# Kernel tuning notes

Measured on AMD Instinct MI355X. Metric: run time of the kernel, lower is better.

Reference implementation:

```python
import jax, jax.numpy as jnp
import numpy as np

B, S, DM, H = 4, 2048, 512, 8
HD = DM // H


def setup_inputs() -> dict:
    key = jax.random.key(0)
    ks = jax.random.split(key, 12)
    x = jax.random.normal(ks[0], (B, S, DM), dtype=jnp.float32)
    # causal lower-triangular mask [B, S, S]
    mask = jnp.broadcast_to(jnp.tril(jnp.ones((S, S), dtype=jnp.int32)), (B, S, S))
    # sorted irregular day offsets (trading-day-like), in days
    days_offset = jnp.sort(
        jax.random.uniform(ks[1], (B, S), dtype=jnp.float32) * 3000.0, axis=-1
    )
    scale = 1.0 / np.sqrt(DM)
    Wq = jax.random.normal(ks[2], (DM, DM), dtype=jnp.float32) * scale
    bq = jnp.zeros((DM,), dtype=jnp.float32)
    Wk = jax.random.normal(ks[3], (DM, DM), dtype=jnp.float32) * scale
    bk = jnp.zeros((DM,), dtype=jnp.float32)
    Wv = jax.random.normal(ks[4], (DM, DM), dtype=jnp.float32) * scale
    bv = jnp.zeros((DM,), dtype=jnp.float32)
    Wo = jax.random.normal(ks[5], (DM, DM), dtype=jnp.float32) * scale
    bo = jnp.zeros((DM,), dtype=jnp.float32)
    decay_rate = jnp.float32(0.1)
    return {
        "x": x, "mask": mask, "days_offset": days_offset,
        "Wq": Wq, "bq": bq, "Wk": Wk, "bk": bk,
        "Wv": Wv, "bv": bv, "Wo": Wo, "bo": bo,
        "decay_rate": decay_rate,
    }


def reference(x, mask, days_offset, Wq, bq, Wk, bk, Wv, bv, Wo, bo, decay_rate):
    b, s, _ = x.shape
    # projections (torch Linear: x @ W.T + b), split heads -> [b, h, s, hd]
    def proj(W, bias):
        return (x @ W.T + bias).reshape(b, s, H, HD).transpose(0, 2, 1, 3)
    q, k, v = proj(Wq, bq), proj(Wk, bk), proj(Wv, bv)
    scores = jnp.einsum("bhqd,bhkd->bhqk", q, k) / jnp.sqrt(jnp.float32(HD))
    # temporal decay: exp(-rate * |t_i - t_j|), broadcast over heads
    dist = jnp.abs(days_offset[:, :, None] - days_offset[:, None, :])  # [b,s,s]
    decay = jnp.exp(-decay_rate * dist)
    scores = scores * decay[:, None, :, :]
    scores = jnp.where(mask[:, None, :, :] == 0, -jnp.inf, scores)
    attn = jax.nn.softmax(scores, axis=-1)  # dropout p=0 (eval)
    out = jnp.einsum("bhqk,bhkd->bhqd", attn, v)
    out = out.transpose(0, 2, 1, 3).reshape(b, s, DM)
    return out @ Wo.T + bo
```

## Files before the change

### kernel.cpp

```cpp
#include <hip/hip_runtime.h>
#include <hip/hip_fp16.h>


#define S_LEN 2048
#define DMODEL 512
#define NH 8
#define HD 64

typedef _Float16 half8 __attribute__((ext_vector_type(8)));
typedef _Float16 half4 __attribute__((ext_vector_type(4)));
typedef float floatx4 __attribute__((ext_vector_type(4)));

__device__ __forceinline__ void gload16(const _Float16* g, _Float16* l) {
    __builtin_amdgcn_global_load_lds(
        (const __attribute__((address_space(1))) void*)g,
        (__attribute__((address_space(3))) void*)l, 16, 0, 0);
}

__global__ __launch_bounds__(256) void cast_f2h(
    const float* __restrict__ x,
    const float* __restrict__ Wq, const float* __restrict__ Wk,
    const float* __restrict__ Wv, const float* __restrict__ Wo,
    _Float16* __restrict__ xh, _Float16* __restrict__ Wh)
{
    const int z = blockIdx.y;
    const float* src;
    _Float16* dst;
    int n;
    if (z == 0) { src = x; dst = xh; n = 8192 * 512; }
    else {
        src = (z == 1) ? Wq : (z == 2) ? Wk : (z == 3) ? Wv : Wo;
        dst = Wh + (z - 1) * 262144;
        n = 262144;
    }
    const int stride = gridDim.x * 256 * 4;
    for (int i = (blockIdx.x * 256 + threadIdx.x) * 4; i < n; i += stride) {
        float4 v = *(const float4*)(src + i);
        half4 h;
        h[0] = (_Float16)v.x; h[1] = (_Float16)v.y;
        h[2] = (_Float16)v.z; h[3] = (_Float16)v.w;
        *(half4*)(dst + i) = h;
    }
}

__global__ __launch_bounds__(256) void qkv_gemm(
    const _Float16* __restrict__ xh, const _Float16* __restrict__ Wh,
    const float* __restrict__ bq, const float* __restrict__ bk, const float* __restrict__ bv,
    _Float16* __restrict__ outh)
{
    __shared__ _Float16 As[2][128 * 64];
    __shared__ _Float16 Ws[2][128 * 64];
    const int t = threadIdx.x;
    const int bm = blockIdx.x, bn = blockIdx.y, z = blockIdx.z;
    const float* bias = (z == 0) ? bq : (z == 1) ? bk : bv;
    const int w = t >> 6, lane = t & 63, l15 = lane & 15, quad = lane >> 4;
    const int wrow = (w >> 1) * 64, wcol = (w & 1) * 64;
    const int lrow = lane >> 3, lane7 = lane & 7;
    const int sw = lane7 ^ lrow;
    const _Float16* xb = xh + (size_t)(bm * 128) * DMODEL;
    const _Float16* Wb = Wh + z * 262144 + (size_t)(bn * 128) * DMODEL;

    auto stage = [&](int kb, int buf) {
        #pragma unroll
        for (int i = 0; i < 4; ++i) {
            const int grp = w * 4 + i;
            const int row = grp * 8 + lrow;
            gload16(xb + (size_t)row * DMODEL + kb * 64 + sw * 8, &As[buf][grp * 512]);
            gload16(Wb + (size_t)row * DMODEL + kb * 64 + sw * 8, &Ws[buf][grp * 512]);
        }
    };

    floatx4 acc[4][4] = {};
    stage(0, 0);
    for (int kb = 0; kb < 8; ++kb) {
        const int buf = kb & 1;
        __syncthreads();
        if (kb < 7) stage(kb + 1, buf ^ 1);
        #pragma unroll
        for (int kk = 0; kk < 2; ++kk) {
            half8 xf[4], wf[4];
            #pragma unroll
            for (int mt = 0; mt < 4; ++mt)
                xf[mt] = *(const half8*)(&As[buf][(wrow + mt * 16 + l15) * 64 + (((quad + 4 * kk) ^ (l15 & 7)) * 8)]);
            #pragma unroll
            for (int nt = 0; nt < 4; ++nt)
                wf[nt] = *(const half8*)(&Ws[buf][(wcol + nt * 16 + l15) * 64 + (((quad + 4 * kk) ^ (l15 & 7)) * 8)]);
            if (z == 2) {
                #pragma unroll
                for (int mt = 0; mt < 4; ++mt)
                    #pragma unroll
                    for (int nt = 0; nt < 4; ++nt)
                        acc[mt][nt] = __builtin_amdgcn_mfma_f32_16x16x32_f16(xf[mt], wf[nt], acc[mt][nt], 0, 0, 0);
            } else {
                #pragma unroll
                for (int nt = 0; nt < 4; ++nt)
                    #pragma unroll
                    for (int mt = 0; mt < 4; ++mt)
                        acc[nt][mt] = __builtin_amdgcn_mfma_f32_16x16x32_f16(wf[nt], xf[mt], acc[nt][mt], 0, 0, 0);
            }
        }
    }

    if (z == 2) {
        #pragma unroll
        for (int mt = 0; mt < 4; ++mt)
            #pragma unroll
            for (int nt = 0; nt < 4; ++nt) {
                int n = bn * 128 + wcol + nt * 16 + l15;
                float bvv = bias[n];
                int m0 = bm * 128 + wrow + mt * 16 + quad * 4;
                int b = m0 >> 11, s0 = m0 & 2047;
                int hh = n >> 6, hd = n & 63;
                half4 hv;
                #pragma unroll
                for (int r = 0; r < 4; ++r) hv[r] = (_Float16)(acc[mt][nt][r] + bvv);
                *(half4*)(outh + (size_t)2 * (8192 * 512) +
                          ((size_t)(b * NH + hh) * HD + hd) * S_LEN + s0) = hv;
            }
    } else {
        #pragma unroll
        for (int nt = 0; nt < 4; ++nt)
            #pragma unroll
            for (int mt = 0; mt < 4; ++mt) {
                int n0 = bn * 128 + wcol + nt * 16 + quad * 4;
                float4 b4 = *(const float4*)(bias + n0);
                int m = bm * 128 + wrow + mt * 16 + l15;
                int b = m >> 11, s = m & 2047;
                int hh = n0 >> 6, hd0 = n0 & 63;
                half4 hv;
                hv[0] = (_Float16)(acc[nt][mt][0] + b4.x);
                hv[1] = (_Float16)(acc[nt][mt][1] + b4.y);
                hv[2] = (_Float16)(acc[nt][mt][2] + b4.z);
                hv[3] = (_Float16)(acc[nt][mt][3] + b4.w);
                *(half4*)(outh + (size_t)z * (8192 * 512) +
                          ((size_t)(b * NH + hh) * S_LEN + s) * HD + hd0) = hv;
            }
    }
}

__global__ __launch_bounds__(256) void out_gemm(
    const _Float16* __restrict__ A, const _Float16* __restrict__ Woh,
    const float* __restrict__ bo, float* __restrict__ outf)
{
    __shared__ _Float16 As[2][64 * 64];
    __shared__ _Float16 Ws[2][128 * 64];
    const int t = threadIdx.x;
    const int bm = blockIdx.x, bn = blockIdx.y;
    const int w = t >> 6, lane = t & 63, l15 = lane & 15, quad = lane >> 4;
    const int wn = w * 32;
    const int lrow = lane >> 3, lane7 = lane & 7;
    const int sw = lane7 ^ lrow;
    const _Float16* Ab = A   + (size_t)(bm * 64) * DMODEL;
    const _Float16* Wb = Woh + (size_t)(bn * 128) * DMODEL;

    auto stage = [&](int kb, int buf) {
        #pragma unroll
        for (int i = 0; i < 2; ++i) {
            const int grp = w * 2 + i;
            const int row = grp * 8 + lrow;
            gload16(Ab + (size_t)row * DMODEL + kb * 64 + sw * 8, &As[buf][grp * 512]);
        }
        #pragma unroll
        for (int i = 0; i < 4; ++i) {
            const int grp = w * 4 + i;
            const int row = grp * 8 + lrow;
            gload16(Wb + (size_t)row * DMODEL + kb * 64 + sw * 8, &Ws[buf][grp * 512]);
        }
    };

    floatx4 acc[2][4] = {};
    stage(0, 0);
    for (int kb = 0; kb < 8; ++kb) {
        const int buf = kb & 1;
        __syncthreads();
        if (kb < 7) stage(kb + 1, buf ^ 1);
        #pragma unroll
        for (int kk = 0; kk < 2; ++kk) {
            half8 wf[2], af[4];
            #pragma unroll
            for (int nt = 0; nt < 2; ++nt)
                wf[nt] = *(const half8*)(&Ws[buf][(wn + nt * 16 + l15) * 64 + (((quad + 4 * kk) ^ (l15 & 7)) * 8)]);
            #pragma unroll
            for (int mt = 0; mt < 4; ++mt)
                af[mt] = *(const half8*)(&As[buf][(mt * 16 + l15) * 64 + (((quad + 4 * kk) ^ (l15 & 7)) * 8)]);
            #pragma unroll
            for (int nt = 0; nt < 2; ++nt)
                #pragma unroll
                for (int mt = 0; mt < 4; ++mt)
                    acc[nt][mt] = __builtin_amdgcn_mfma_f32_16x16x32_f16(wf[nt], af[mt], acc[nt][mt], 0, 0, 0);
        }
    }

    #pragma unroll
    for (int nt = 0; nt < 2; ++nt)
        #pragma unroll
        for (int mt = 0; mt < 4; ++mt) {
            int n0 = bn * 128 + wn + nt * 16 + quad * 4;
            float4 b4 = *(const float4*)(bo + n0);
            int m = bm * 64 + mt * 16 + l15;
            float4 v;
            v.x = acc[nt][mt][0] + b4.x; v.y = acc[nt][mt][1] + b4.y;
            v.z = acc[nt][mt][2] + b4.z; v.w = acc[nt][mt][3] + b4.w;
            *(float4*)(outf + (size_t)m * DMODEL + n0) = v;
        }
}

__global__ __launch_bounds__(256, 2) void attn_k(
    const _Float16* __restrict__ Qh, const _Float16* __restrict__ Kh,
    const _Float16* __restrict__ Vt, const float* __restrict__ days,
    const float* __restrict__ rate_p, _Float16* __restrict__ Ah)
{
    __shared__ _Float16 Ks[2][64 * 64];
    __shared__ _Float16 Vs[2][64 * 64];
    __shared__ float    eks[2][64];
    __shared__ float4   PsRaw[1024];
    __shared__ float    lred[2][2][64];

    _Float16* Ps  = (_Float16*)PsRaw;
    float*    PsF = (float*)PsRaw;

    const int h = blockIdx.x, pr = blockIdx.y, b = blockIdx.z;
    const int t = threadIdx.x, w = t >> 6, lane = t & 63;
    const int l15 = lane & 15, quad = lane >> 4, e7 = l15 & 7;
    const int qh = w & 1, kh = w >> 1;
    const float rate = rate_p[0];
    const size_t bhoff = (size_t)(b * NH + h) * (size_t)(S_LEN * HD);
    const _Float16* Qb = Qh + bhoff;
    const _Float16* Kb = Kh + bhoff;
    const _Float16* Vb = Vt + bhoff;
    const float* daysb = days + b * S_LEN;
    const int lrow = lane >> 3, sw = (lane & 7) ^ lrow;

    auto stage = [&](int kt, int buf) {
        #pragma unroll
        for (int i = 0; i < 2; ++i) {
            int grp = w * 2 + i;
            int row = grp * 8 + lrow;
            gload16(Kb + (size_t)(kt * 64 + row) * HD + sw * 8, &Ks[buf][grp * 512]);
            gload16(Vb + (size_t)row * S_LEN + kt * 64 + sw * 8, &Vs[buf][grp * 512]);
        }
        if (w == 0) {
            float tk0 = daysb[kt * 64];
            float d = daysb[kt * 64 + lane];
            eks[buf][lane] = __expf(fminf(rate * (d - tk0), 80.f));
        }
    };

    auto run_phase = [&](int j, int par0, int nextj) -> int {
        const int q0 = j * 64 + qh * 32;
        half8 qf[2][2];
        #pragma unroll
        for (int qc = 0; qc < 2; ++qc)
            #pragma unroll
            for (int kk = 0; kk < 2; ++kk)
                qf[qc][kk] = *(const half8*)(Qb + (size_t)(q0 + qc * 16 + l15) * HD + kk * 32 + quad * 8);

        const int   qg[2] = {q0 + l15, q0 + 16 + l15};
        const float tq[2] = {daysb[qg[0]], daysb[qg[1]]};

        floatx4 oacc[2][4] = {};
        float lacc[2] = {0.f, 0.f};

        floatx4 scA[2][2], scB[2][2];
        half8  vfA[4], vfB[4];
        floatx4 ekA[2], ekB[2];
        float  eqA[2], eqB[2];

        auto load_tile = [&](int kt, int par, floatx4 (&sc)[2][2], half8 (&vf)[4],
                             floatx4 (&ek)[2], float (&eq)[2]) {
            half8 kf[2][2];
            #pragma unroll
            for (int c = 0; c < 2; ++c) {
                const int C = kh * 2 + c;
                #pragma unroll
                for (int kk = 0; kk < 2; ++kk)
                    kf[c][kk] = *(const half8*)(&Ks[par][(C * 16 + l15) * 64 + (((quad + 4 * kk) ^ e7) * 8)]);
            }
            #pragma unroll
            for (int qc = 0; qc < 2; ++qc)
                #pragma unroll
                for (int c = 0; c < 2; ++c) {
                    floatx4 z = {};
                    z = __builtin_amdgcn_mfma_f32_16x16x32_f16(kf[c][0], qf[qc][0], z, 0, 0, 0);
                    sc[qc][c] = __builtin_amdgcn_mfma_f32_16x16x32_f16(kf[c][1], qf[qc][1], z, 0, 0, 0);
                }
            #pragma unroll
            for (int s4 = 0; s4 < 4; ++s4)
                vf[s4] = *(const half8*)(&Vs[par][(s4 * 16 + l15) * 64 + (((quad + 4 * kh) ^ e7) * 8)]);
            const float tk0 = daysb[kt * 64];
            #pragma unroll
            for (int qc = 0; qc < 2; ++qc)
                eq[qc] = 0.125f * __expf(-rate * (tq[qc] - tk0));
            #pragma unroll
            for (int c = 0; c < 2; ++c)
                ek[c] = *(const floatx4*)(&eks[par][kh * 32 + c * 16 + quad * 4]);
        };

        auto softmax_pv = [&](floatx4 (&sc)[2][2], half8 (&vf)[4],
                              floatx4 (&ek)[2], float (&eq)[2], bool dg, int kt) {
            #pragma unroll
            for (int qc = 0; qc < 2; ++qc)
                #pragma unroll
                for (int c = 0; c < 2; ++c) {
                    float pv[4];
                    #pragma unroll
                    for (int r = 0; r < 4; ++r) {
                        float p = __expf(sc[qc][c][r] * (eq[qc] * ek[c][r]));
                        if (dg && (kt * 64 + kh * 32 + c * 16 + quad * 4 + r) > qg[qc]) p = 0.f;
                        lacc[qc] += p;
                        pv[r] = p;
                    }
                    half4 hv;
                    hv[0] = (_Float16)pv[0]; hv[1] = (_Float16)pv[1];
                    hv[2] = (_Float16)pv[2]; hv[3] = (_Float16)pv[3];
                    *(half4*)(&Ps[(w * 2 + qc) * 1024 + l15 * 64 +
                                  (((kh * 4 + 2 * c + (quad >> 1)) ^ e7) * 8) + (quad & 1) * 4]) = hv;
                }
            #pragma unroll
            for (int qc = 0; qc < 2; ++qc) {
                half8 pf = *(const half8*)(&Ps[(w * 2 + qc) * 1024 + l15 * 64 + (((quad + 4 * kh) ^ e7) * 8)]);
                #pragma unroll
                for (int s4 = 0; s4 < 4; ++s4)
                    oacc[qc][s4] = __builtin_amdgcn_mfma_f32_16x16x32_f16(vf[s4], pf, oacc[qc][s4], 0, 0, 0);
            }
        };

        __syncthreads();
        if (j > 0) stage(1, par0 ^ 1);
        load_tile(0, par0, scA, vfA, ekA, eqA);

        int kt = 1;
        for (; kt + 1 <= j; kt += 2) {
            const int p1 = (par0 + kt) & 1;
            __syncthreads();
            if (kt < j) stage(kt + 1, p1 ^ 1);
            load_tile(kt, p1, scB, vfB, ekB, eqB);
            softmax_pv(scA, vfA, ekA, eqA, false, kt - 1);
            const int p2 = p1 ^ 1;
            __syncthreads();
            if (kt + 1 < j) stage(kt + 2, p2 ^ 1);
            load_tile(kt + 1, p2, scA, vfA, ekA, eqA);
            softmax_pv(scB, vfB, ekB, eqB, false, kt);
        }
        if (kt <= j) {
            const int p1 = (par0 + kt) & 1;
            __syncthreads();
            load_tile(kt, p1, scB, vfB, ekB, eqB);
            softmax_pv(scA, vfA, ekA, eqA, false, kt - 1);
            softmax_pv(scB, vfB, ekB, eqB, true, j);
        } else {
            softmax_pv(scA, vfA, ekA, eqA, true, j);
        }

        __syncthreads();
        if (w >= 2) {
            #pragma unroll
            for (int qc = 0; qc < 2; ++qc) {
                #pragma unroll
                for (int s4 = 0; s4 < 4; ++s4)
                    *(floatx4*)(&PsF[(((w & 1) * 2 + qc) * 4 + s4) * 256 + lane * 4]) = oacc[qc][s4];
                lred[w & 1][qc][lane] = lacc[qc];
            }
        }
        __syncthreads();
        const int parNext = (par0 + j + 1) & 1;
        if (nextj >= 0) stage(0, parNext);
        if (w < 2) {
            #pragma unroll
            for (int qc = 0; qc < 2; ++qc) {
                float l = lacc[qc] + lred[w][qc][lane];
                l += __shfl_xor(l, 16);
                l += __shfl_xor(l, 32);
                const float linv = 1.0f / l;
                #pragma unroll
                for (int s4 = 0; s4 < 4; ++s4) {
                    floatx4 o = oacc[qc][s4] +
                        *(const floatx4*)(&PsF[((w * 2 + qc) * 4 + s4) * 256 + lane * 4]);
                    half4 hv;
                    #pragma unroll
                    for (int r = 0; r < 4; ++r) hv[r] = (_Float16)(o[r] * linv);
                    *(half4*)(Ah + ((size_t)(b * S_LEN) + qg[qc]) * DMODEL + h * HD + s4 * 16 + quad * 4) = hv;
                }
            }
        }
        return parNext;
    };

    const int j0 = pr, j1 = 31 - pr;
    stage(0, 0);
    int p1 = run_phase(j0, 0, j1);
    run_phase(j1, p1, -1);
}

extern "C" void kernel_launch(void* const* d_in, const int* in_sizes, int n_in,
                              void* d_out, int out_size, void* d_ws, size_t ws_size,
                              hipStream_t stream)
{
    const float* x    = (const float*)d_in[0];
    const float* days = (const float*)d_in[2];
    const float* Wq   = (const float*)d_in[3];
    const float* bq   = (const float*)d_in[4];
    const float* Wk   = (const float*)d_in[5];
    const float* bk   = (const float*)d_in[6];
    const float* Wv   = (const float*)d_in[7];
    const float* bv   = (const float*)d_in[8];
    const float* Wo   = (const float*)d_in[9];
    const float* bo   = (const float*)d_in[10];
    const float* rate = (const float*)d_in[11];
    float* out = (float*)d_out;

    _Float16* Qh  = (_Float16*)d_ws;
    _Float16* Kh  = Qh + 4194304;
    _Float16* Vh  = Kh + 4194304;
    _Float16* AhX = Vh + 4194304;
    _Float16* Wh  = AhX + 4194304;

    dim3 gc(512, 5, 1);
    cast_f2h<<<gc, 256, 0, stream>>>(x, Wq, Wk, Wv, Wo, AhX, Wh);

    dim3 g0(64, 4, 3);
    qkv_gemm<<<g0, 256, 0, stream>>>(AhX, Wh, bq, bk, bv, Qh);

    dim3 ga(NH, 16, 4);
    attn_k<<<ga, 256, 0, stream>>>(Qh, Kh, Vh, days, rate, AhX);

    dim3 g1(128, 4, 1);
    out_gemm<<<g1, 256, 0, stream>>>(AhX, Wh + 3 * 262144, bo, out);
}
```

Baseline: 203.3 us.

## Use 512-thread blocks covering 128 query rows, dropping paired-phase load balancing

After: 331.6 us. +63.1%, slower.

```diff
diff --git a/kernel.cpp b/kernel.cpp
--- a/kernel.cpp
+++ b/kernel.cpp
@@ -205,7 +205,7 @@
         }
 }
 
-__global__ __launch_bounds__(256, 2) void attn_k(
+__global__ __launch_bounds__(512, 4) void attn_k(
     const _Float16* __restrict__ Qh, const _Float16* __restrict__ Kh,
     const _Float16* __restrict__ Vt, const float* __restrict__ days,
     const float* __restrict__ rate_p, _Float16* __restrict__ Ah)
@@ -213,16 +213,18 @@
     __shared__ _Float16 Ks[2][64 * 64];
     __shared__ _Float16 Vs[2][64 * 64];
     __shared__ float    eks[2][64];
-    __shared__ float4   PsRaw[1024];
-    __shared__ float    lred[2][2][64];
+    __shared__ float4   PsRaw[2048];
+    __shared__ float    lred[4][2][64];
 
     _Float16* Ps  = (_Float16*)PsRaw;
     float*    PsF = (float*)PsRaw;
 
-    const int h = blockIdx.x, pr = blockIdx.y, b = blockIdx.z;
+    const int h = blockIdx.x, b = blockIdx.y;
+    const int j = 15 - blockIdx.z;
     const int t = threadIdx.x, w = t >> 6, lane = t & 63;
     const int l15 = lane & 15, quad = lane >> 4, e7 = l15 & 7;
-    const int qh = w & 1, kh = w >> 1;
+    const int qq = w >> 1, kh = w & 1;
+    const int nt = 2 * j + 2;
     const float rate = rate_p[0];
     const size_t bhoff = (size_t)(b * NH + h) * (size_t)(S_LEN * HD);
     const _Float16* Qb = Qh + bhoff;
@@ -232,13 +234,9 @@
     const int lrow = lane >> 3, sw = (lane & 7) ^ lrow;
 
     auto stage = [&](int kt, int buf) {
-        #pragma unroll
-        for (int i = 0; i < 2; ++i) {
-            int grp = w * 2 + i;
-            int row = grp * 8 + lrow;
-            gload16(Kb + (size_t)(kt * 64 + row) * HD + sw * 8, &Ks[buf][grp * 512]);
-            gload16(Vb + (size_t)row * S_LEN + kt * 64 + sw * 8, &Vs[buf][grp * 512]);
-        }
+        const int row = w * 8 + lrow;
+        gload16(Kb + (size_t)(kt * 64 + row) * HD + sw * 8, &Ks[buf][w * 512]);
+        gload16(Vb + (size_t)row * S_LEN + kt * 64 + sw * 8, &Vs[buf][w * 512]);
         if (w == 0) {
             float tk0 = daysb[kt * 64];
             float d = daysb[kt * 64 + lane];
@@ -246,150 +244,139 @@
         }
     };
 
-    auto run_phase = [&](int j, int par0, int nextj) -> int {
-        const int q0 = j * 64 + qh * 32;
-        half8 qf[2][2];
+    const int q0 = j * 128 + qq * 32;
+    half8 qf[2][2];
+    #pragma unroll
+    for (int qc = 0; qc < 2; ++qc)
+        #pragma unroll
+        for (int kk = 0; kk < 2; ++kk)
+            qf[qc][kk] = *(const half8*)(Qb + (size_t)(q0 + qc * 16 + l15) * HD + kk * 32 + quad * 8);
+
+    const int   qg[2] = {q0 + l15, q0 + 16 + l15};
+    const float tq[2] = {daysb[qg[0]], daysb[qg[1]]};
+
+    floatx4 oacc[2][4] = {};
+    float lacc[2] = {0.f, 0.f};
+
+    floatx4 scA[2][2], scB[2][2];
+    half8  vfA[4], vfB[4];
+    floatx4 ekA[2], ekB[2];
+    float  eqA[2], eqB[2];
+
+    auto load_tile = [&](int kt, int par, floatx4 (&sc)[2][2], half8 (&vf)[4],
+                         floatx4 (&ek)[2], float (&eq)[2]) {
+        half8 kf[2][2];
+        #pragma unroll
+        for (int c = 0; c < 2; ++c) {
+            const int C = kh * 2 + c;
+            #pragma unroll
+            for (int kk = 0; kk < 2; ++kk)
+                kf[c][kk] = *(const half8*)(&Ks[par][(C * 16 + l15) * 64 + (((quad + 4 * kk) ^ e7) * 8)]);
+        }
         #pragma unroll
         for (int qc = 0; qc < 2; ++qc)
             #pragma unroll
-            for (int kk = 0; kk < 2; ++kk)
-                qf[qc][kk] = *(const half8*)(Qb + (size_t)(q0 + qc * 16 + l15) * HD + kk * 32 + quad * 8);
-
-        const int   qg[2] = {q0 + l15, q0 + 16 + l15};
-        const float tq[2] = {daysb[qg[0]], daysb[qg[1]]};
-
-        floatx4 oacc[2][4] = {};
-        float lacc[2] = {0.f, 0.f};
-
-        floatx4 scA[2][2], scB[2][2];
-        half8  vfA[4], vfB[4];
-        floatx4 ekA[2], ekB[2];
-        float  eqA[2], eqB[2];
-
-        auto load_tile = [&](int kt, int par, floatx4 (&sc)[2][2], half8 (&vf)[4],
-                             floatx4 (&ek)[2], float (&eq)[2]) {
-            half8 kf[2][2];
-            #pragma unroll
             for (int c = 0; c < 2; ++c) {
-                const int C = kh * 2 + c;
-                #pragma unroll
-                for (int kk = 0; kk < 2; ++kk)
-                    kf[c][kk] = *(const half8*)(&Ks[par][(C * 16 + l15) * 64 + (((quad + 4 * kk) ^ e7) * 8)]);
-            }
-            #pragma unroll
-            for (int qc = 0; qc < 2; ++qc)
-                #pragma unroll
-                for (int c = 0; c < 2; ++c) {
-                    floatx4 z = {};
-                    z = __builtin_amdgcn_mfma_f32_16x16x32_f16(kf[c][0], qf[qc][0], z, 0, 0, 0);
-                    sc[qc][c] = __builtin_amdgcn_mfma_f32_16x16x32_f16(kf[c][1], qf[qc][1], z, 0, 0, 0);
+                floatx4 z = {};
+                z = __builtin_amdgcn_mfma_f32_16x16x32_f16(kf[c][0], qf[qc][0], z, 0, 0, 0);
+                sc[qc][c] = __builtin_amdgcn_mfma_f32_16x16x32_f16(kf[c][1], qf[qc][1], z, 0, 0, 0);
+            }
+        #pragma unroll
+        for (int s4 = 0; s4 < 4; ++s4)
+            vf[s4] = *(const half8*)(&Vs[par][(s4 * 16 + l15) * 64 + (((quad + 4 * kh) ^ e7) * 8)]);
+        const float tk0 = daysb[kt * 64];
+        #pragma unroll
+        for (int qc = 0; qc < 2; ++qc)
+            eq[qc] = 0.125f * __expf(-rate * (tq[qc] - tk0));
+        #pragma unroll
+        for (int c = 0; c < 2; ++c)
+            ek[c] = *(const floatx4*)(&eks[par][kh * 32 + c * 16 + quad * 4]);
+    };
+
+    auto softmax_pv = [&](floatx4 (&sc)[2][2], half8 (&vf)[4],
+                          floatx4 (&ek)[2], float (&eq)[2], bool dg, int kt) {
+        #pragma unroll
+        for (int qc = 0; qc < 2; ++qc)
+            #pragma unroll
+            for (int c = 0; c < 2; ++c) {
+                float pv[4];
+                #pragma unroll
+                for (int r = 0; r < 4; ++r) {
+                    float p = __expf(sc[qc][c][r] * (eq[qc] * ek[c][r]));
+                    if (dg && (kt * 64 + kh * 32 + c * 16 + quad * 4 + r) > qg[qc]) p = 0.f;
+                    lacc[qc] += p;
+                    pv[r] = p;
                 }
+                half4 hv;
+                hv[0] = (_Float16)pv[0]; hv[1] = (_Float16)pv[1];
+                hv[2] = (_Float16)pv[2]; hv[3] = (_Float16)pv[3];
+                *(half4*)(&Ps[(w * 2 + qc) * 1024 + l15 * 64 +
+                              (((kh * 4 + 2 * c + (quad >> 1)) ^ e7) * 8) + (quad & 1) * 4]) = hv;
+            }
+        #pragma unroll
+        for (int qc = 0; qc < 2; ++qc) {
+            half8 pf = *(const half8*)(&Ps[(w * 2 + qc) * 1024 + l15 * 64 + (((quad + 4 * kh) ^ e7) * 8)]);
             #pragma unroll
             for (int s4 = 0; s4 < 4; ++s4)
-                vf[s4] = *(const half8*)(&Vs[par][(s4 * 16 + l15) * 64 + (((quad + 4 * kh) ^ e7) * 8)]);
-            const float tk0 = daysb[kt * 64];
-            #pragma unroll
-            for (int qc = 0; qc < 2; ++qc)
-                eq[qc] = 0.125f * __expf(-rate * (tq[qc] - tk0));
-            #pragma unroll
-            for (int c = 0; c < 2; ++c)
-                ek[c] = *(const floatx4*)(&eks[par][kh * 32 + c * 16 + quad * 4]);
-        };
-
-        auto softmax_pv = [&](floatx4 (&sc)[2][2], half8 (&vf)[4],
-                              floatx4 (&ek)[2], float (&eq)[2], bool dg, int kt) {
-            #pragma unroll
-            for (int qc = 0; qc < 2; ++qc)
-                #pragma unroll
-                for (int c = 0; c < 2; ++c) {
-                    float pv[4];
-                    #pragma unroll
-                    for (int r = 0; r < 4; ++r) {
-                        float p = __expf(sc[qc][c][r] * (eq[qc] * ek[c][r]));
-                        if (dg && (kt * 64 + kh * 32 + c * 16 + quad * 4 + r) > qg[qc]) p = 0.f;
-                        lacc[qc] += p;
-                        pv[r] = p;
-                    }
-                    half4 hv;
-                    hv[0] = (_Float16)pv[0]; hv[1] = (_Float16)pv[1];
-                    hv[2] = (_Float16)pv[2]; hv[3] = (_Float16)pv[3];
-                    *(half4*)(&Ps[(w * 2 + qc) * 1024 + l15 * 64 +
-                                  (((kh * 4 + 2 * c + (quad >> 1)) ^ e7) * 8) + (quad & 1) * 4]) = hv;
-                }
-            #pragma unroll
-            for (int qc = 0; qc < 2; ++qc) {
-                half8 pf = *(const half8*)(&Ps[(w * 2 + qc) * 1024 + l15 * 64 + (((quad + 4 * kh) ^ e7) * 8)]);
-                #pragma unroll
-                for (int s4 = 0; s4 < 4; ++s4)
-                    oacc[qc][s4] = __builtin_amdgcn_mfma_f32_16x16x32_f16(vf[s4], pf, oacc[qc][s4], 0, 0, 0);
-            }
-        };
-
+                oacc[qc][s4] = __builtin_amdgcn_mfma_f32_16x16x32_f16(vf[s4], pf, oacc[qc][s4], 0, 0, 0);
+        }
+    };
+
+    stage(0, 0);
+    __syncthreads();
+    if (nt > 1) stage(1, 1);
+    load_tile(0, 0, scA, vfA, ekA, eqA);
+
+    int kt = 1;
+    for (; kt + 1 < nt; kt += 2) {
+        const int p1 = kt & 1;
         __syncthreads();
-        if (j > 0) stage(1, par0 ^ 1);
-        load_tile(0, par0, scA, vfA, ekA, eqA);
-
-        int kt = 1;
-        for (; kt + 1 <= j; kt += 2) {
-            const int p1 = (par0 + kt) & 1;
-            __syncthreads();
-            if (kt < j) stage(kt + 1, p1 ^ 1);
-            load_tile(kt, p1, scB, vfB, ekB, eqB);
-            softmax_pv(scA, vfA, ekA, eqA, false, kt - 1);
-            const int p2 = p1 ^ 1;
-            __syncthreads();
-            if (kt + 1 < j) stage(kt + 2, p2 ^ 1);
-            load_tile(kt + 1, p2, scA, vfA, ekA, eqA);
-            softmax_pv(scB, vfB, ekB, eqB, false, kt);
-        }
-        if (kt <= j) {
-            const int p1 = (par0 + kt) & 1;
-            __syncthreads();
-            load_tile(kt, p1, scB, vfB, ekB, eqB);
-            softmax_pv(scA, vfA, ekA, eqA, false, kt - 1);
-            softmax_pv(scB, vfB, ekB, eqB, true, j);
-        } else {
-            softmax_pv(scA, vfA, ekA, eqA, true, j);
-        }
-
+        stage(kt + 1, p1 ^ 1);
+        load_tile(kt, p1, scB, vfB, ekB, eqB);
+        softmax_pv(scA, vfA, ekA, eqA, (kt - 1) >= nt - 2, kt - 1);
+        const int p2 = p1 ^ 1;
         __syncthreads();
-        if (w >= 2) {
-            #pragma unroll
-            for (int qc = 0; qc < 2; ++qc) {
-                #pragma unroll
-                for (int s4 = 0; s4 < 4; ++s4)
-                    *(floatx4*)(&PsF[(((w & 1) * 2 + qc) * 4 + s4) * 256 + lane * 4]) = oacc[qc][s4];
-                lred[w & 1][qc][lane] = lacc[qc];
-            }
-        }
+        if (kt + 2 < nt) stage(kt + 2, p2 ^ 1);
+        load_tile(kt + 1, p2, scA, vfA, ekA, eqA);
+        softmax_pv(scB, vfB, ekB, eqB, kt >= nt - 2, kt);
+    }
+    {
+        const int p1 = kt & 1;
         __syncthreads();
-        const int parNext = (par0 + j + 1) & 1;
-        if (nextj >= 0) stage(0, parNext);
-        if (w < 2) {
-            #pragma unroll
-            for (int qc = 0; qc < 2; ++qc) {
-                float l = lacc[qc] + lred[w][qc][lane];
-                l += __shfl_xor(l, 16);
-                l += __shfl_xor(l, 32);
-                const float linv = 1.0f / l;
-                #pragma unroll
-                for (int s4 = 0; s4 < 4; ++s4) {
-                    floatx4 o = oacc[qc][s4] +
-                        *(const floatx4*)(&PsF[((w * 2 + qc) * 4 + s4) * 256 + lane * 4]);
-                    half4 hv;
-                    #pragma unroll
-                    for (int r = 0; r < 4; ++r) hv[r] = (_Float16)(o[r] * linv);
-                    *(half4*)(Ah + ((size_t)(b * S_LEN) + qg[qc]) * DMODEL + h * HD + s4 * 16 + quad * 4) = hv;
-                }
-            }
-        }
-        return parNext;
-    };
-
-    const int j0 = pr, j1 = 31 - pr;
-    stage(0, 0);
-    int p1 = run_phase(j0, 0, j1);
-    run_phase(j1, p1, -1);
+        load_tile(kt, p1, scB, vfB, ekB, eqB);
+        softmax_pv(scA, vfA, ekA, eqA, (kt - 1) >= nt - 2, kt - 1);
+        softmax_pv(scB, vfB, ekB, eqB, true, kt);
+    }
+
+    __syncthreads();
+    if (kh == 1) {
+        #pragma unroll
+        for (int qc = 0; qc < 2; ++qc) {
+            #pragma unroll
+            for (int s4 = 0; s4 < 4; ++s4)
+                *(floatx4*)(&PsF[((qq * 2 + qc) * 4 + s4) * 256 + lane * 4]) = oacc[qc][s4];
+            lred[qq][qc][lane] = lacc[qc];
+        }
+    }
+    __syncthreads();
+    if (kh == 0) {
+        #pragma unroll
+        for (int qc = 0; qc < 2; ++qc) {
+            float l = lacc[qc] + lred[qq][qc][lane];
+            l += __shfl_xor(l, 16);
+            l += __shfl_xor(l, 32);
+            const float linv = 1.0f / l;
+            #pragma unroll
+            for (int s4 = 0; s4 < 4; ++s4) {
+                floatx4 o = oacc[qc][s4] +
+                    *(const floatx4*)(&PsF[((qq * 2 + qc) * 4 + s4) * 256 + lane * 4]);
+                half4 hv;
+                #pragma unroll
+                for (int r = 0; r < 4; ++r) hv[r] = (_Float16)(o[r] * linv);
+                *(half4*)(Ah + ((size_t)(b * S_LEN) + qg[qc]) * DMODEL + h * HD + s4 * 16 + quad * 4) = hv;
+            }
+        }
+    }
 }
 
 extern "C" void kernel_launch(void* const* d_in, const int* in_sizes, int n_in,
@@ -421,8 +408,8 @@
     dim3 g0(64, 4, 3);
     qkv_gemm<<<g0, 256, 0, stream>>>(AhX, Wh, bq, bk, bv, Qh);
 
-    dim3 ga(NH, 16, 4);
-    attn_k<<<ga, 256, 0, stream>>>(Qh, Kh, Vh, days, rate, AhX);
+    dim3 ga(NH, 4, 16);
+    attn_k<<<ga, 512, 0, stream>>>(Qh, Kh, Vh, days, rate, AhX);
 
     dim3 g1(128, 4, 1);
     out_gemm<<<g1, 256, 0, stream>>>(AhX, Wh + 3 * 262144, bo, out);
```

## Triple-buffer attention K/V tiles with counted waits and one q-tile per block

Applied to the files above, without the earlier changes.

After: 202.6 us. Within noise of the previous version (-0.3%).

```diff
diff --git a/kernel.cpp b/kernel.cpp
--- a/kernel.cpp
+++ b/kernel.cpp
@@ -210,16 +210,19 @@
     const _Float16* __restrict__ Vt, const float* __restrict__ days,
     const float* __restrict__ rate_p, _Float16* __restrict__ Ah)
 {
-    __shared__ _Float16 Ks[2][64 * 64];
-    __shared__ _Float16 Vs[2][64 * 64];
-    __shared__ float    eks[2][64];
+    __shared__ _Float16 Ks[3][64 * 64];
+    __shared__ _Float16 Vs[3][64 * 64];
+    __shared__ float    eks_all[2048];
+    __shared__ float    tk0s[32];
     __shared__ float4   PsRaw[1024];
     __shared__ float    lred[2][2][64];
 
     _Float16* Ps  = (_Float16*)PsRaw;
     float*    PsF = (float*)PsRaw;
 
-    const int h = blockIdx.x, pr = blockIdx.y, b = blockIdx.z;
+    const int h = blockIdx.x, b = blockIdx.y;
+    const int j = 31 - blockIdx.z;
+    const int nt = j + 1;
     const int t = threadIdx.x, w = t >> 6, lane = t & 63;
     const int l15 = lane & 15, quad = lane >> 4, e7 = l15 & 7;
     const int qh = w & 1, kh = w >> 1;
@@ -239,157 +242,175 @@
             gload16(Kb + (size_t)(kt * 64 + row) * HD + sw * 8, &Ks[buf][grp * 512]);
             gload16(Vb + (size_t)row * S_LEN + kt * 64 + sw * 8, &Vs[buf][grp * 512]);
         }
-        if (w == 0) {
-            float tk0 = daysb[kt * 64];
-            float d = daysb[kt * 64 + lane];
-            eks[buf][lane] = __expf(fminf(rate * (d - tk0), 80.f));
-        }
-    };
-
-    auto run_phase = [&](int j, int par0, int nextj) -> int {
-        const int q0 = j * 64 + qh * 32;
-        half8 qf[2][2];
+    };
+
+    auto sync_cnt = [&](bool counted) {
+        if (counted) asm volatile("s_waitcnt vmcnt(4) lgkmcnt(0)" ::: "memory");
+        else         asm volatile("s_waitcnt vmcnt(0) lgkmcnt(0)" ::: "memory");
+        __builtin_amdgcn_s_barrier();
+        __builtin_amdgcn_sched_barrier(0);
+    };
+
+    stage(0, 0);
+    if (nt > 1) stage(1, 1);
+    {
+        const int k0 = t * 8;
+        if (k0 < nt * 64) {
+            const float anchor = daysb[k0 & ~63];
+            float4 d0 = *(const float4*)(daysb + k0);
+            float4 d1 = *(const float4*)(daysb + k0 + 4);
+            eks_all[k0 + 0] = __expf(fminf(rate * (d0.x - anchor), 80.f));
+            eks_all[k0 + 1] = __expf(fminf(rate * (d0.y - anchor), 80.f));
+            eks_all[k0 + 2] = __expf(fminf(rate * (d0.z - anchor), 80.f));
+            eks_all[k0 + 3] = __expf(fminf(rate * (d0.w - anchor), 80.f));
+            eks_all[k0 + 4] = __expf(fminf(rate * (d1.x - anchor), 80.f));
+            eks_all[k0 + 5] = __expf(fminf(rate * (d1.y - anchor), 80.f));
+            eks_all[k0 + 6] = __expf(fminf(rate * (d1.z - anchor), 80.f));
+            eks_all[k0 + 7] = __expf(fminf(rate * (d1.w - anchor), 80.f));
+        }
+        if (t < 32) tk0s[t] = daysb[t * 64];
+    }
+
+    const int q0 = j * 64 + qh * 32;
+    half8 qf[2][2];
+    #pragma unroll
+    for (int qc = 0; qc < 2; ++qc)
+        #pragma unroll
+        for (int kk = 0; kk < 2; ++kk)
+            qf[qc][kk] = *(const half8*)(Qb + (size_t)(q0 + qc * 16 + l15) * HD + kk * 32 + quad * 8);
+
+    const int   qg[2] = {q0 + l15, q0 + 16 + l15};
+    const float tq[2] = {daysb[qg[0]], daysb[qg[1]]};
+
+    __syncthreads();
+
+    floatx4 oacc[2][4] = {};
+    float lacc[2] = {0.f, 0.f};
+
+    floatx4 scA[2][2], scB[2][2];
+    half8  vfA[4], vfB[4];
+    floatx4 ekA[2], ekB[2];
+    float  eqA[2], eqB[2];
+
+    auto load_tile = [&](int kt, int par, floatx4 (&sc)[2][2], half8 (&vf)[4],
+                         floatx4 (&ek)[2], float (&eq)[2]) {
+        half8 kf[2][2];
+        #pragma unroll
+        for (int c = 0; c < 2; ++c) {
+            const int C = kh * 2 + c;
+            #pragma unroll
+            for (int kk = 0; kk < 2; ++kk)
+                kf[c][kk] = *(const half8*)(&Ks[par][(C * 16 + l15) * 64 + (((quad + 4 * kk) ^ e7) * 8)]);
+        }
         #pragma unroll
         for (int qc = 0; qc < 2; ++qc)
             #pragma unroll
-            for (int kk = 0; kk < 2; ++kk)
-                qf[qc][kk] = *(const half8*)(Qb + (size_t)(q0 + qc * 16 + l15) * HD + kk * 32 + quad * 8);
-
-        const int   qg[2] = {q0 + l15, q0 + 16 + l15};
-        const float tq[2] = {daysb[qg[0]], daysb[qg[1]]};
-
-        floatx4 oacc[2][4] = {};
-        float lacc[2] = {0.f, 0.f};
-
-        floatx4 scA[2][2], scB[2][2];
-        half8  vfA[4], vfB[4];
-        floatx4 ekA[2], ekB[2];
-        float  eqA[2], eqB[2];
-
-        auto load_tile = [&](int kt, int par, floatx4 (&sc)[2][2], half8 (&vf)[4],
-                             floatx4 (&ek)[2], float (&eq)[2]) {
-            half8 kf[2][2];
-            #pragma unroll
             for (int c = 0; c < 2; ++c) {
-                const int C = kh * 2 + c;
-                #pragma unroll
-                for (int kk = 0; kk < 2; ++kk)
-                    kf[c][kk] = *(const half8*)(&Ks[par][(C * 16 + l15) * 64 + (((quad + 4 * kk) ^ e7) * 8)]);
-            }
-            #pragma unroll
-            for (int qc = 0; qc < 2; ++qc)
-                #pragma unroll
-                for (int c = 0; c < 2; ++c) {
-                    floatx4 z = {};
-                    z = __builtin_amdgcn_mfma_f32_16x16x32_f16(kf[c][0], qf[qc][0], z, 0, 0, 0);
-                    sc[qc][c] = __builtin_amdgcn_mfma_f32_16x16x32_f16(kf[c][1], qf[qc][1], z, 0, 0, 0);
+                floatx4 z = {};
+                z = __builtin_amdgcn_mfma_f32_16x16x32_f16(kf[c][0], qf[qc][0], z, 0, 0, 0);
+                sc[qc][c] = __builtin_amdgcn_mfma_f32_16x16x32_f16(kf[c][1], qf[qc][1], z, 0, 0, 0);
+            }
+        #pragma unroll
+        for (int s4 = 0; s4 < 4; ++s4)
+            vf[s4] = *(const half8*)(&Vs[par][(s4 * 16 + l15) * 64 + (((quad + 4 * kh) ^ e7) * 8)]);
+        const float tk0 = tk0s[kt];
+        #pragma unroll
+        for (int qc = 0; qc < 2; ++qc)
+            eq[qc] = 0.125f * __expf(-rate * (tq[qc] - tk0));
+        #pragma unroll
+        for (int c = 0; c < 2; ++c)
+            ek[c] = *(const floatx4*)(&eks_all[kt * 64 + kh * 32 + c * 16 + quad * 4]);
+    };
+
+    auto softmax_pv = [&](floatx4 (&sc)[2][2], half8 (&vf)[4],
+                          floatx4 (&ek)[2], float (&eq)[2], bool dg, int kt) {
+        #pragma unroll
+        for (int qc = 0; qc < 2; ++qc)
+            #pragma unroll
+            for (int c = 0; c < 2; ++c) {
+                float pv[4];
+                #pragma unroll
+                for (int r = 0; r < 4; ++r) {
+                    float p = __expf(sc[qc][c][r] * (eq[qc] * ek[c][r]));
+                    if (dg && (kt * 64 + kh * 32 + c * 16 + quad * 4 + r) > qg[qc]) p = 0.f;
+                    lacc[qc] += p;
+                    pv[r] = p;
                 }
+                half4 hv;
+                hv[0] = (_Float16)pv[0]; hv[1] = (_Float16)pv[1];
+                hv[2] = (_Float16)pv[2]; hv[3] = (_Float16)pv[3];
+                *(half4*)(&Ps[(w * 2 + qc) * 1024 + l15 * 64 +
+                              (((kh * 4 + 2 * c + (quad >> 1)) ^ e7) * 8) + (quad & 1) * 4]) = hv;
+            }
+        #pragma unroll
+        for (int qc = 0; qc < 2; ++qc) {
+            half8 pf = *(const half8*)(&Ps[(w * 2 + qc) * 1024 + l15 * 64 + (((quad + 4 * kh) ^ e7) * 8)]);
             #pragma unroll
             for (int s4 = 0; s4 < 4; ++s4)
-                vf[s4] = *(const half8*)(&Vs[par][(s4 * 16 + l15) * 64 + (((quad + 4 * kh) ^ e7) * 8)]);
-            const float tk0 = daysb[kt * 64];
-            #pragma unroll
-            for (int qc = 0; qc < 2; ++qc)
-                eq[qc] = 0.125f * __expf(-rate * (tq[qc] - tk0));
-            #pragma unroll
-            for (int c = 0; c < 2; ++c)
-                ek[c] = *(const floatx4*)(&eks[par][kh * 32 + c * 16 + quad * 4]);
-        };
-
-        auto softmax_pv = [&](floatx4 (&sc)[2][2], half8 (&vf)[4],
-                              floatx4 (&ek)[2], float (&eq)[2], bool dg, int kt) {
-            #pragma unroll
-            for (int qc = 0; qc < 2; ++qc)
-                #pragma unroll
-                for (int c = 0; c < 2; ++c) {
-                    float pv[4];
-                    #pragma unroll
-                    for (int r = 0; r < 4; ++r) {
-                        float p = __expf(sc[qc][c][r] * (eq[qc] * ek[c][r]));
-                        if (dg && (kt * 64 + kh * 32 + c * 16 + quad * 4 + r) > qg[qc]) p = 0.f;
-                        lacc[qc] += p;
-                        pv[r] = p;
-                    }
-                    half4 hv;
-                    hv[0] = (_Float16)pv[0]; hv[1] = (_Float16)pv[1];
-                    hv[2] = (_Float16)pv[2]; hv[3] = (_Float16)pv[3];
-                    *(half4*)(&Ps[(w * 2 + qc) * 1024 + l15 * 64 +
-                                  (((kh * 4 + 2 * c + (quad >> 1)) ^ e7) * 8) + (quad & 1) * 4]) = hv;
-                }
-            #pragma unroll
-            for (int qc = 0; qc < 2; ++qc) {
-                half8 pf = *(const half8*)(&Ps[(w * 2 + qc) * 1024 + l15 * 64 + (((quad + 4 * kh) ^ e7) * 8)]);
-                #pragma unroll
-                for (int s4 = 0; s4 < 4; ++s4)
-                    oacc[qc][s4] = __builtin_amdgcn_mfma_f32_16x16x32_f16(vf[s4], pf, oacc[qc][s4], 0, 0, 0);
-            }
-        };
-
-        __syncthreads();
-        if (j > 0) stage(1, par0 ^ 1);
-        load_tile(0, par0, scA, vfA, ekA, eqA);
-
-        int kt = 1;
-        for (; kt + 1 <= j; kt += 2) {
-            const int p1 = (par0 + kt) & 1;
-            __syncthreads();
-            if (kt < j) stage(kt + 1, p1 ^ 1);
-            load_tile(kt, p1, scB, vfB, ekB, eqB);
-            softmax_pv(scA, vfA, ekA, eqA, false, kt - 1);
-            const int p2 = p1 ^ 1;
-            __syncthreads();
-            if (kt + 1 < j) stage(kt + 2, p2 ^ 1);
-            load_tile(kt + 1, p2, scA, vfA, ekA, eqA);
-            softmax_pv(scB, vfB, ekB, eqB, false, kt);
-        }
-        if (kt <= j) {
-            const int p1 = (par0 + kt) & 1;
-            __syncthreads();
-            load_tile(kt, p1, scB, vfB, ekB, eqB);
-            softmax_pv(scA, vfA, ekA, eqA, false, kt - 1);
-            softmax_pv(scB, vfB, ekB, eqB, true, j);
-        } else {
-            softmax_pv(scA, vfA, ekA, eqA, true, j);
-        }
-
-        __syncthreads();
-        if (w >= 2) {
-            #pragma unroll
-            for (int qc = 0; qc < 2; ++qc) {
-                #pragma unroll
-                for (int s4 = 0; s4 < 4; ++s4)
-                    *(floatx4*)(&PsF[(((w & 1) * 2 + qc) * 4 + s4) * 256 + lane * 4]) = oacc[qc][s4];
-                lred[w & 1][qc][lane] = lacc[qc];
-            }
-        }
-        __syncthreads();
-        const int parNext = (par0 + j + 1) & 1;
-        if (nextj >= 0) stage(0, parNext);
-        if (w < 2) {
-            #pragma unroll
-            for (int qc = 0; qc < 2; ++qc) {
-                float l = lacc[qc] + lred[w][qc][lane];
-                l += __shfl_xor(l, 16);
-                l += __shfl_xor(l, 32);
-                const float linv = 1.0f / l;
-                #pragma unroll
-                for (int s4 = 0; s4 < 4; ++s4) {
-                    floatx4 o = oacc[qc][s4] +
-                        *(const floatx4*)(&PsF[((w * 2 + qc) * 4 + s4) * 256 + lane * 4]);
-                    half4 hv;
-                    #pragma unroll
-                    for (int r = 0; r < 4; ++r) hv[r] = (_Float16)(o[r] * linv);
-                    *(half4*)(Ah + ((size_t)(b * S_LEN) + qg[qc]) * DMODEL + h * HD + s4 * 16 + quad * 4) = hv;
-                }
-            }
-        }
-        return parNext;
-    };
-
-    const int j0 = pr, j1 = 31 - pr;
-    stage(0, 0);
-    int p1 = run_phase(j0, 0, j1);
-    run_phase(j1, p1, -1);
+                oacc[qc][s4] = __builtin_amdgcn_mfma_f32_16x16x32_f16(vf[s4], pf, oacc[qc][s4], 0, 0, 0);
+        }
+    };
+
+    load_tile(0, 0, scA, vfA, ekA, eqA);
+    if (nt > 2) stage(2, 2);
+    sync_cnt(nt > 2);
+
+    int kt = 1;
+    int bB = 1;
+    for (; kt + 1 < nt; kt += 2) {
+        const int bA = (bB == 2) ? 0 : bB + 1;
+        const int b2 = (bB == 0) ? 2 : bB - 1;
+
+        load_tile(kt, bB, scB, vfB, ekB, eqB);
+        softmax_pv(scA, vfA, ekA, eqA, false, kt - 1);
+        if (kt + 2 < nt) stage(kt + 2, b2);
+        sync_cnt(kt + 2 < nt);
+
+        load_tile(kt + 1, bA, scA, vfA, ekA, eqA);
+        softmax_pv(scB, vfB, ekB, eqB, false, kt);
+        if (kt + 3 < nt) stage(kt + 3, bB);
+        sync_cnt(kt + 3 < nt);
+
+        bB = b2;
+    }
+
+    if (kt < nt) {
+        load_tile(kt, bB, scB, vfB, ekB, eqB);
+        softmax_pv(scA, vfA, ekA, eqA, false, kt - 1);
+        softmax_pv(scB, vfB, ekB, eqB, true, kt);
+    } else {
+        softmax_pv(scA, vfA, ekA, eqA, true, nt - 1);
+    }
+
+    __syncthreads();
+    if (kh == 1) {
+        #pragma unroll
+        for (int qc = 0; qc < 2; ++qc) {
+            #pragma unroll
+            for (int s4 = 0; s4 < 4; ++s4)
+                *(floatx4*)(&PsF[((qh * 2 + qc) * 4 + s4) * 256 + lane * 4]) = oacc[qc][s4];
+            lred[qh][qc][lane] = lacc[qc];
+        }
+    }
+    __syncthreads();
+    if (kh == 0) {
+        #pragma unroll
+        for (int qc = 0; qc < 2; ++qc) {
+            float l = lacc[qc] + lred[qh][qc][lane];
+            l += __shfl_xor(l, 16);
+            l += __shfl_xor(l, 32);
+            const float linv = 1.0f / l;
+            #pragma unroll
+            for (int s4 = 0; s4 < 4; ++s4) {
+                floatx4 o = oacc[qc][s4] +
+                    *(const floatx4*)(&PsF[((qh * 2 + qc) * 4 + s4) * 256 + lane * 4]);
+                half4 hv;
+                #pragma unroll
+                for (int r = 0; r < 4; ++r) hv[r] = (_Float16)(o[r] * linv);
+                *(half4*)(Ah + ((size_t)(b * S_LEN) + qg[qc]) * DMODEL + h * HD + s4 * 16 + quad * 4) = hv;
+            }
+        }
+    }
 }
 
 extern "C" void kernel_launch(void* const* d_in, const int* in_sizes, int n_in,
@@ -421,7 +442,7 @@
     dim3 g0(64, 4, 3);
     qkv_gemm<<<g0, 256, 0, stream>>>(AhX, Wh, bq, bk, bv, Qh);
 
-    dim3 ga(NH, 16, 4);
+    dim3 ga(NH, 4, 32);
     attn_k<<<ga, 256, 0, stream>>>(Qh, Kh, Vh, days, rate, AhX);
 
     dim3 g1(128, 4, 1);
```
